# Performance work log

Measured on AMD Instinct MI355X. Metric: run time of the kernel, lower is better.

## Reference

```python
import jax, jax.numpy as jnp
import numpy as np

IMAGE_TOKEN_INDEX = -200
B, N, D = 2, 768, 2048          # batch, seq, llm_size
CLIP = 1024                      # clip hidden size
NUM_HEADS = 8
HEAD_DIM = CLIP // NUM_HEADS
NUM_LAYER, LAYER_RATE = 24, 4
LAYER_IDX = np.asarray(NUM_LAYER - np.arange(0, NUM_LAYER + 1, LAYER_RATE))  # [24,20,16,12,8,4,0]
J = len(LAYER_IDX)               # 7 selected layers
L = NUM_LAYER + 1                # 25 stacked layers in all_features
IMG, PATCH = 336, 14
HP = IMG // PATCH                # 24 patches per side; patch_ratio == 1
HW = HP * HP                     # 576 vision tokens
SL = HP * (HP + 1) + 1           # 601 = H*(W+1)+1 ragged slice length
SCALE = CLIP ** (-0.5)
LN_EPS = 1e-5
COS_EPS = 1e-8


def setup_inputs() -> dict:
    key = jax.random.key(0)
    ks = jax.random.split(key, 10)
    input_ids = jax.random.randint(ks[0], (B, N), 0, 32000)
    pos = jnp.array([37, 111])  # image-token positions; pos + SL <= N
    input_ids = input_ids.at[jnp.arange(B), pos].set(IMAGE_TOKEN_INDEX)
    rgb = jax.random.normal(ks[1], (B, 3, IMG, IMG), dtype=jnp.float32)
    mask = jnp.ones((B, 1, IMG, IMG), dtype=jnp.float32)  # last channel: all-ones mask
    images = jnp.concatenate([rgb, mask], axis=1)
    all_features = jax.random.normal(ks[2], (B, N, L, D), dtype=jnp.float32)
    patch_hw = jnp.full((B, 2), HP, dtype=jnp.int32)
    s = 0.02
    return {
        'input_ids': input_ids,
        'images': images,
        'all_features': all_features,
        'patch_hw': patch_hw,
        'norm_gamma': jnp.ones((J, D), dtype=jnp.float32),
        'norm_beta': jnp.zeros((J, D), dtype=jnp.float32),
        'norm_w': jax.random.normal(ks[3], (J, CLIP, D), dtype=jnp.float32) * s,
        'input_w': jax.random.normal(ks[4], (CLIP, D), dtype=jnp.float32) * s,
        'input_b': jnp.zeros((CLIP,), dtype=jnp.float32),
        'output_w': jax.random.normal(ks[5], (CLIP, CLIP), dtype=jnp.float32) * s,
        'output_b': jnp.zeros((CLIP,), dtype=jnp.float32),
        'clip_w': jax.random.normal(ks[6], (CLIP, 3 * PATCH * PATCH), dtype=jnp.float32) * s,
        'clip_b': jnp.zeros((CLIP,), dtype=jnp.float32),
    }


def reference(input_ids, images, all_features, patch_hw,
              norm_gamma, norm_beta, norm_w,
              input_w, input_b, output_w, output_b, clip_w, clip_b):
    # clip_layer modeled as a frozen 14x14 patch-embed linear -> [B, HW, CLIP]
    patches = images[:, :3].reshape(B, 3, HP, PATCH, HP, PATCH)
    patches = patches.transpose(0, 2, 4, 1, 3, 5).reshape(B, HW, 3 * PATCH * PATCH)
    clip_feats = patches @ clip_w.T + clip_b  # [B, HW, CLIP]
    # mask channel is all ones -> pooled clip_2d_mask keeps every patch
    lidx = jnp.asarray(LAYER_IDX)

    def per_sample(ids, feats, cf):
        # ragged slice at the image token (data-dependent start, fixed length)
        idx = jnp.argmax(ids == IMAGE_TOKEN_INDEX)
        f = jax.lax.dynamic_slice_in_dim(feats, idx, SL, axis=0)[1:]      # [600, L, D]
        # [L,D,H,W+1] drop-last-col in torch == row-major split here
        f = f.reshape(HP, HP + 1, L, D)[:, :HP].reshape(HW, L, D)          # [576, L, D]
        # per-layer LayerNorm + no-bias Linear on 7 selected layers
        xj = f[:, lidx]                                                    # [HW, J, D]
        mu = xj.mean(-1, keepdims=True)
        var = ((xj - mu) ** 2).mean(-1, keepdims=True)
        xn = (xj - mu) / jnp.sqrt(var + LN_EPS) * norm_gamma + norm_beta
        vis = jnp.einsum('njd,jcd->njc', xn, norm_w)                       # [HW, J, CLIP]
        inp = f[:, -1] @ input_w.T + input_b                               # [HW, CLIP]
        # single-query multi-head cross attention over the J-1 kv layers
        q = vis[:, 0].reshape(HW, NUM_HEADS, HEAD_DIM)                     # [HW, h, d]
        kv = vis[:, 1:].reshape(HW, J - 1, NUM_HEADS, HEAD_DIM).transpose(0, 2, 1, 3)  # [HW, h, J-1, d]
        attn = jax.nn.softmax((q[:, :, None, :] * SCALE * kv).sum(-1), axis=-1)        # [HW, h, J-1]
        fuse = (attn[..., None] * kv).sum(-2).reshape(HW, CLIP)
        out = inp + fuse @ output_w.T + output_b                           # [HW, CLIP]
        denom = jnp.maximum(jnp.linalg.norm(out, axis=-1) * jnp.linalg.norm(cf, axis=-1), COS_EPS)
        cos = (out * cf).sum(-1) / denom
        return 1.0 - cos.mean()

    losses = jax.vmap(per_sample)(input_ids, all_features, clip_feats)
    return losses.mean()  # mse_loss / count_image with count_image == B
```

## Files before the change

kernel.cpp:

```cpp
#include <hip/hip_runtime.h>

#define HW_   576
#define BHW   1152
#define DD    2048
#define CLIPC 1024
#define NSEQ  768
#define LL    25
#define KPAD  640

typedef __bf16 bf16x8 __attribute__((ext_vector_type(8)));
typedef float  f32x4  __attribute__((ext_vector_type(4)));
typedef unsigned short u16;

__device__ __forceinline__ float bf2f(u16 u){
  union { unsigned int i; float f; } v; v.i = ((unsigned int)u) << 16; return v.f;
}
__device__ __forceinline__ u16 f2bf(float f){
  union { float f; unsigned int i; } v; v.f = f;
  unsigned int u = v.i;
  return (u16)((u + 0x7fffu + ((u >> 16) & 1u)) >> 16);
}

__device__ __forceinline__ void gld_lds16(const void* g, void* l){
  __builtin_amdgcn_global_load_lds((__attribute__((address_space(1))) void*)g,
                                   (__attribute__((address_space(3))) void*)l,
                                   16, 0, 0);
}

__global__ void setup_k(const int* __restrict__ ids, int* __restrict__ idxbuf,
                        float* __restrict__ rowacc){
  const int lane = threadIdx.x;
  for (int b = 0; b < 2; b++){
    int best = 0x7fffffff;
    for (int i = lane; i < NSEQ; i += 64)
      if (ids[b*NSEQ + i] == -200 && i < best) best = i;
    for (int off = 32; off; off >>= 1){ int o = __shfl_xor(best, off); best = min(best, o); }
    if (lane == 0) idxbuf[b] = best;
  }
  for (int i = lane; i < BHW*4; i += 64) rowacc[i] = 0.f;
}

__global__ void prep_k(const float* __restrict__ norm_w, const float* __restrict__ input_w,
                       const float* __restrict__ output_w, const float* __restrict__ clip_w,
                       const float* __restrict__ images, const float* __restrict__ feats,
                       const int* __restrict__ idxbuf,
                       const float* __restrict__ gamma, const float* __restrict__ beta,
                       u16* __restrict__ B_all, u16* __restrict__ outw,
                       u16* __restrict__ clipw, u16* __restrict__ patch,
                       u16* __restrict__ A_all){
  const int blk = blockIdx.x, tid = threadIdx.x;
  if (blk < 17408){
    const long n1 = 7L*CLIPC*DD, n2 = (long)CLIPC*DD;
    long idx = ((long)blk*256 + tid) * 4;
    const float* s; u16* d;
    if (idx < n1)         { s = norm_w  + idx;              d = B_all + idx; }
    else if (idx < n1+n2) { s = input_w + (idx - n1);       d = B_all + idx; }
    else                  { s = output_w + (idx - n1 - n2); d = outw + (idx - n1 - n2); }
    float4 v = *(const float4*)s;
    union { u16 u[4]; unsigned long long q; } pk;
    pk.u[0] = f2bf(v.x); pk.u[1] = f2bf(v.y); pk.u[2] = f2bf(v.z); pk.u[3] = f2bf(v.w);
    *(unsigned long long*)d = pk.q;
    return;
  }
  if (blk < 18432){
    const int c = blk - 17408;
    for (int k = tid; k < KPAD; k += 256)
      clipw[c*KPAD + k] = (k < 588) ? f2bf(clip_w[c*588 + k]) : (u16)0;
    return;
  }
  if (blk < 19584){
    const int r = blk - 18432;
    const int b = r / HW_, n = r % HW_;
    const int hi = n / 24, wi = n % 24;
    for (int p = tid; p < KPAD; p += 256){
      float v = 0.f;
      if (p < 588){
        int c3 = p / 196, rem = p - c3*196;
        int ph = rem / 14, pw = rem - ph*14;
        v = images[(((long)b*4 + c3)*336 + hi*14 + ph)*336 + wi*14 + pw];
      }
      patch[(long)r*KPAD + p] = f2bf(v);
    }
    return;
  }
  const int q = blk - 19584;
  const int r = q >> 3, g = q & 7;
  const int b = r / HW_, n = r % HW_;
  const int hi = n / 24, wi = n % 24;
  const int tok = idxbuf[b] + 1 + hi*25 + wi;
  const int layer = (g < 7) ? (24 - g*4) : 24;
  const float* src = feats + (((long)(b*NSEQ + tok))*LL + layer)*DD;
  float v[8];
#pragma unroll
  for (int k = 0; k < 8; k++) v[k] = src[tid + k*256];
  u16* dst = A_all + ((long)g*BHW + r)*DD;
  if (g == 7){
#pragma unroll
    for (int k = 0; k < 8; k++) dst[tid + k*256] = f2bf(v[k]);
    return;
  }
  float s = 0.f, qq = 0.f;
#pragma unroll
  for (int k = 0; k < 8; k++){ s += v[k]; qq += v[k]*v[k]; }
  for (int off = 32; off; off >>= 1){ s += __shfl_xor(s, off); qq += __shfl_xor(qq, off); }
  __shared__ float rs[4], rq[4];
  const int wave = tid >> 6, lane = tid & 63;
  if (lane == 0){ rs[wave] = s; rq[wave] = qq; }
  __syncthreads();
  const float ts = rs[0]+rs[1]+rs[2]+rs[3];
  const float tq = rq[0]+rq[1]+rq[2]+rq[3];
  const float mu   = ts * (1.f/2048.f);
  const float var  = tq * (1.f/2048.f) - mu*mu;
  const float rstd = rsqrtf(var + 1e-5f);
  const float* gm = gamma + g*DD;
  const float* bt = beta  + g*DD;
#pragma unroll
  for (int k = 0; k < 8; k++){
    int d = tid + k*256;
    dst[d] = f2bf((v[k]-mu)*rstd*gm[d] + bt[d]);
  }
}

__device__ __forceinline__ void gemm_core(const u16* __restrict__ Az, const u16* __restrict__ Bz,
                                          int K, int bm, int bn,
                                          u16* __restrict__ As, u16* __restrict__ Bs,
                                          f32x4 (&acc)[4][4]){
  const int tid  = threadIdx.x;
  const int wave = tid >> 6, lane = tid & 63;
  const int l15 = lane & 15, quad = lane >> 4;
  const int wr = (wave >> 1) * 64, wc = (wave & 1) * 64;
  const int laneRow = lane >> 3;
  const int laneCol = (((lane & 7) ^ laneRow) * 8);
  const u16* gA = Az + (long)(bm + wave*32 + laneRow)*K + laneCol;
  const u16* gB = Bz + (long)(bn + wave*32 + laneRow)*K + laneCol;
  u16* lA = &As[wave*2048];
  u16* lB = &Bs[wave*2048];
  const long rs8 = (long)8 * K;

  for (int k0 = 0; k0 < K; k0 += 64){
#pragma unroll
    for (int t = 0; t < 4; t++) gld_lds16(gA + k0 + t*rs8, lA + t*512);
#pragma unroll
    for (int t = 0; t < 4; t++) gld_lds16(gB + k0 + t*rs8, lB + t*512);
    __syncthreads();
#pragma unroll
    for (int s = 0; s < 2; s++){
      bf16x8 af[4], bg[4];
#pragma unroll
      for (int i = 0; i < 4; i++)
        af[i] = *(const bf16x8*)&As[(wr + i*16 + l15)*64 + (((s*4 + quad) ^ (l15 & 7)) * 8)];
#pragma unroll
      for (int j = 0; j < 4; j++)
        bg[j] = *(const bf16x8*)&Bs[(wc + j*16 + l15)*64 + (((s*4 + quad) ^ (l15 & 7)) * 8)];
#pragma unroll
      for (int i = 0; i < 4; i++)
#pragma unroll
        for (int j = 0; j < 4; j++)
          acc[i][j] = __builtin_amdgcn_mfma_f32_16x16x32_bf16(af[i], bg[j], acc[i][j], 0, 0, 0);
    }
    __syncthreads();
  }
}

__global__ __launch_bounds__(256, 3)
void gemm9_k(const u16* __restrict__ A_all, const u16* __restrict__ B_all,
             u16* __restrict__ C_all, const u16* __restrict__ patch,
             const u16* __restrict__ clipw, float* __restrict__ cf,
             const float* __restrict__ input_b, const float* __restrict__ clip_b){
  __shared__ alignas(16) u16 As[128*64];
  __shared__ alignas(16) u16 Bs[128*64];
  const int z = blockIdx.z;
  const int bm = blockIdx.x * 128, bn = blockIdx.y * 128;
  const u16 *Az, *Bz; int K;
  if (z < 8){ Az = A_all + (long)z*BHW*DD; Bz = B_all + (long)z*CLIPC*DD; K = DD; }
  else      { Az = patch; Bz = clipw; K = KPAD; }

  f32x4 acc[4][4] = {};
  gemm_core(Az, Bz, K, bm, bn, As, Bs, acc);

  const int lane = threadIdx.x & 63, wave = threadIdx.x >> 6;
  const int l15 = lane & 15, quad = lane >> 4;
  const int wr = (wave >> 1) * 64, wc = (wave & 1) * 64;

  if (z == 8){
#pragma unroll
    for (int i = 0; i < 4; i++)
#pragma unroll
      for (int j = 0; j < 4; j++)
#pragma unroll
        for (int rr = 0; rr < 4; rr++){
          const int row = bm + wr + i*16 + quad*4 + rr;
          const int col = bn + wc + j*16 + l15;
          cf[(long)row*CLIPC + col] = acc[i][j][rr] + clip_b[col];
        }
  } else {
    u16* C = C_all + (long)z*BHW*CLIPC;
    const bool do_bias = (z == 7);
#pragma unroll
    for (int i = 0; i < 4; i++)
#pragma unroll
      for (int j = 0; j < 4; j++)
#pragma unroll
        for (int rr = 0; rr < 4; rr++){
          const int row = bm + wr + i*16 + quad*4 + rr;
          const int col = bn + wc + j*16 + l15;
          float v = acc[i][j][rr];
          if (do_bias) v += input_b[col];
          C[(long)row*CLIPC + col] = f2bf(v);
        }
  }
}

__global__ void attn_k(const u16* __restrict__ C_all, u16* __restrict__ fuse){
  const int r = blockIdx.x;
  const int h = (blockIdx.y << 2) | (threadIdx.x >> 6);
  const int lane = threadIdx.x & 63;
  const long slot = (long)BHW * CLIPC;
  const long rb = (long)r * CLIPC;
  const int c0 = h*128 + lane, c1 = c0 + 64;
  const float q0 = bf2f(C_all[rb + c0]), q1 = bf2f(C_all[rb + c1]);
  float k0v[6], k1v[6], dt[6];
#pragma unroll
  for (int t = 0; t < 6; t++){
    const u16* base = C_all + (long)(t+1)*slot + rb;
    k0v[t] = bf2f(base[c0]); k1v[t] = bf2f(base[c1]);
    dt[t] = q0*k0v[t] + q1*k1v[t];
  }
#pragma unroll
  for (int t = 0; t < 6; t++)
    for (int off = 32; off; off >>= 1) dt[t] += __shfl_xor(dt[t], off);
  float l[6], e[6];
#pragma unroll
  for (int t = 0; t < 6; t++) l[t] = dt[t] * 0.03125f;
  float m = l[0];
#pragma unroll
  for (int t = 1; t < 6; t++) m = fmaxf(m, l[t]);
  float ssum = 0.f;
#pragma unroll
  for (int t = 0; t < 6; t++){ e[t] = __expf(l[t] - m); ssum += e[t]; }
  const float inv = 1.f / ssum;
  float f0 = 0.f, f1 = 0.f;
#pragma unroll
  for (int t = 0; t < 6; t++){ const float a = e[t]*inv; f0 += a*k0v[t]; f1 += a*k1v[t]; }
  fuse[rb + c0] = f2bf(f0);
  fuse[rb + c1] = f2bf(f1);
}

__global__ __launch_bounds__(256, 3)
void gemm_out_k(const u16* __restrict__ fuse, const u16* __restrict__ outw,
                const u16* __restrict__ inp, const float* __restrict__ output_b,
                const float* __restrict__ cf, float* __restrict__ rowacc){
  __shared__ alignas(16) u16 As[128*64];
  __shared__ alignas(16) u16 Bs[128*64];
  const int bm = blockIdx.x * 128, bn = blockIdx.y * 128;
  f32x4 acc[4][4] = {};
  gemm_core(fuse, outw, CLIPC, bm, bn, As, Bs, acc);

  const int lane = threadIdx.x & 63, wave = threadIdx.x >> 6;
  const int l15 = lane & 15, quad = lane >> 4;
  const int wr = (wave >> 1) * 64, wc = (wave & 1) * 64;

#pragma unroll
  for (int i = 0; i < 4; i++)
#pragma unroll
    for (int rr = 0; rr < 4; rr++){
      const int row = bm + wr + i*16 + quad*4 + rr;
      float soc = 0.f, soo = 0.f, scc = 0.f;
#pragma unroll
      for (int j = 0; j < 4; j++){
        const int col = bn + wc + j*16 + l15;
        const long p = (long)row*CLIPC + col;
        const float o = acc[i][j][rr] + output_b[col] + bf2f(inp[p]);
        const float c = cf[p];
        soc += o*c; soo += o*o; scc += c*c;
      }
#pragma unroll
      for (int off = 1; off < 16; off <<= 1){
        soc += __shfl_xor(soc, off); soo += __shfl_xor(soo, off); scc += __shfl_xor(scc, off);
      }
      if (l15 == 0){
        atomicAdd(&rowacc[row*4 + 0], soc);
        atomicAdd(&rowacc[row*4 + 1], soo);
        atomicAdd(&rowacc[row*4 + 2], scc);
      }
    }
}

__global__ void fin_k(const float* __restrict__ rowacc, float* __restrict__ out){
  const int tid = threadIdx.x;
  float s = 0.f;
  for (int r = tid; r < BHW; r += 256){
    const float soc = rowacc[r*4], soo = rowacc[r*4+1], scc = rowacc[r*4+2];
    s += soc / fmaxf(sqrtf(soo*scc), 1e-8f);
  }
  for (int off = 32; off; off >>= 1) s += __shfl_xor(s, off);
  __shared__ float rs[4];
  const int wave = tid >> 6, lane = tid & 63;
  if (lane == 0) rs[wave] = s;
  __syncthreads();
  if (tid == 0) out[0] = 1.f - (rs[0]+rs[1]+rs[2]+rs[3]) * (1.f/(float)BHW);
}

extern "C" void kernel_launch(void* const* d_in, const int* in_sizes, int n_in,
                              void* d_out, int out_size, void* d_ws, size_t ws_size,
                              hipStream_t stream){
  const int*   input_ids = (const int*)  d_in[0];
  const float* images    = (const float*)d_in[1];
  const float* all_feats = (const float*)d_in[2];
  const float* norm_gamma = (const float*)d_in[4];
  const float* norm_beta  = (const float*)d_in[5];
  const float* norm_w     = (const float*)d_in[6];
  const float* input_w    = (const float*)d_in[7];
  const float* input_b    = (const float*)d_in[8];
  const float* output_w   = (const float*)d_in[9];
  const float* output_b   = (const float*)d_in[10];
  const float* clip_w     = (const float*)d_in[11];
  const float* clip_b     = (const float*)d_in[12];
  float* out = (float*)d_out;

  char* w = (char*)d_ws;
  int*   idxbuf = (int*)w;
  size_t off = 256;
  u16* A_all = (u16*)(w + off); off += 8L*BHW*DD*2;
  u16* B_all = (u16*)(w + off); off += 8L*CLIPC*DD*2;
  u16* C_all = (u16*)(w + off); off += 8L*BHW*CLIPC*2;
  u16* outw  = (u16*)(w + off); off += (long)CLIPC*CLIPC*2;
  u16* clipw = (u16*)(w + off); off += (long)CLIPC*KPAD*2;
  u16* patch = (u16*)(w + off); off += (long)BHW*KPAD*2;
  u16* fuse  = (u16*)(w + off); off += (long)BHW*CLIPC*2;
  float* cf     = (float*)(w + off); off += (long)BHW*CLIPC*4;
  float* rowacc = (float*)(w + off); off += (long)BHW*4*4;

  setup_k<<<1, 64, 0, stream>>>(input_ids, idxbuf, rowacc);
  prep_k<<<28800, 256, 0, stream>>>(norm_w, input_w, output_w, clip_w, images, all_feats,
                                    idxbuf, norm_gamma, norm_beta,
                                    B_all, outw, clipw, patch, A_all);
  gemm9_k<<<dim3(9, 8, 9), 256, 0, stream>>>(A_all, B_all, C_all, patch, clipw, cf,
                                             input_b, clip_b);
  attn_k<<<dim3(1152, 2), 256, 0, stream>>>(C_all, fuse);
  gemm_out_k<<<dim3(9, 8), 256, 0, stream>>>(fuse, outw, C_all + 7L*BHW*CLIPC,
                                             output_b, cf, rowacc);
  fin_k<<<1, 256, 0, stream>>>(rowacc, out);
}
```

Measured before the change: 579.9 us.

## Run the seven layer-norm projections as scaled FP8 MFMA GEMMs

```diff
diff --git a/kernel.cpp b/kernel.cpp
--- a/kernel.cpp
+++ b/kernel.cpp
@@ -8,9 +8,15 @@
 #define LL    25
 #define KPAD  640
 
+#define ASCALE 8.0f
+#define BSCALE 32.0f
+#define INV_AB (1.0f/256.0f)
+
 typedef __bf16 bf16x8 __attribute__((ext_vector_type(8)));
 typedef float  f32x4  __attribute__((ext_vector_type(4)));
+typedef int    i32x8  __attribute__((ext_vector_type(8)));
 typedef unsigned short u16;
+typedef unsigned char  u8;
 
 __device__ __forceinline__ float bf2f(u16 u){
   union { unsigned int i; float f; } v; v.i = ((unsigned int)u) << 16; return v.f;
@@ -19,6 +25,15 @@
   union { float f; unsigned int i; } v; v.f = f;
   unsigned int u = v.i;
   return (u16)((u + 0x7fffu + ((u >> 16) & 1u)) >> 16);
+}
+__device__ __forceinline__ unsigned int pk2bf(float a, float b){
+  return ((unsigned int)f2bf(a)) | (((unsigned int)f2bf(b)) << 16);
+}
+__device__ __forceinline__ unsigned int pk4_fp8(float a, float b, float c, float d){
+  int v = 0;
+  v = __builtin_amdgcn_cvt_pk_fp8_f32(a, b, v, false);
+  v = __builtin_amdgcn_cvt_pk_fp8_f32(c, d, v, true);
+  return (unsigned int)v;
 }
 
 __device__ __forceinline__ void gld_lds16(const void* g, void* l){
@@ -45,31 +60,38 @@
                        const float* __restrict__ images, const float* __restrict__ feats,
                        const int* __restrict__ idxbuf,
                        const float* __restrict__ gamma, const float* __restrict__ beta,
-                       u16* __restrict__ B_all, u16* __restrict__ outw,
+                       u8* __restrict__ B8, u16* __restrict__ inpw, u16* __restrict__ outw,
                        u16* __restrict__ clipw, u16* __restrict__ patch,
-                       u16* __restrict__ A_all){
+                       u8* __restrict__ A8, u16* __restrict__ A7){
   const int blk = blockIdx.x, tid = threadIdx.x;
-  if (blk < 17408){
-    const long n1 = 7L*CLIPC*DD, n2 = (long)CLIPC*DD;
-    long idx = ((long)blk*256 + tid) * 4;
-    const float* s; u16* d;
-    if (idx < n1)         { s = norm_w  + idx;              d = B_all + idx; }
-    else if (idx < n1+n2) { s = input_w + (idx - n1);       d = B_all + idx; }
-    else                  { s = output_w + (idx - n1 - n2); d = outw + (idx - n1 - n2); }
-    float4 v = *(const float4*)s;
-    union { u16 u[4]; unsigned long long q; } pk;
-    pk.u[0] = f2bf(v.x); pk.u[1] = f2bf(v.y); pk.u[2] = f2bf(v.z); pk.u[3] = f2bf(v.w);
-    *(unsigned long long*)d = pk.q;
+  if (blk < 7168){
+    long idx = (long)blk*2048 + tid*8;
+    float4 v0 = *(const float4*)(norm_w + idx);
+    float4 v1 = *(const float4*)(norm_w + idx + 4);
+    uint2 o;
+    o.x = pk4_fp8(v0.x*BSCALE, v0.y*BSCALE, v0.z*BSCALE, v0.w*BSCALE);
+    o.y = pk4_fp8(v1.x*BSCALE, v1.y*BSCALE, v1.z*BSCALE, v1.w*BSCALE);
+    *(uint2*)(B8 + idx) = o;
     return;
   }
-  if (blk < 18432){
-    const int c = blk - 17408;
+  if (blk < 8704){
+    const bool isInp = (blk < 8192);
+    long idx = (long)(blk - (isInp ? 7168 : 8192))*2048 + tid*8;
+    const float* s = isInp ? (input_w + idx) : (output_w + idx);
+    float4 v0 = *(const float4*)s;
+    float4 v1 = *(const float4*)(s + 4);
+    uint4 o = { pk2bf(v0.x,v0.y), pk2bf(v0.z,v0.w), pk2bf(v1.x,v1.y), pk2bf(v1.z,v1.w) };
+    *(uint4*)((isInp ? inpw : outw) + idx) = o;
+    return;
+  }
+  if (blk < 9728){
+    const int c = blk - 8704;
     for (int k = tid; k < KPAD; k += 256)
       clipw[c*KPAD + k] = (k < 588) ? f2bf(clip_w[c*588 + k]) : (u16)0;
     return;
   }
-  if (blk < 19584){
-    const int r = blk - 18432;
+  if (blk < 10880){
+    const int r = blk - 9728;
     const int b = r / HW_, n = r % HW_;
     const int hi = n / 24, wi = n % 24;
     for (int p = tid; p < KPAD; p += 256){
@@ -83,25 +105,22 @@
     }
     return;
   }
-  const int q = blk - 19584;
+  const int q = blk - 10880;
   const int r = q >> 3, g = q & 7;
   const int b = r / HW_, n = r % HW_;
   const int hi = n / 24, wi = n % 24;
   const int tok = idxbuf[b] + 1 + hi*25 + wi;
   const int layer = (g < 7) ? (24 - g*4) : 24;
-  const float* src = feats + (((long)(b*NSEQ + tok))*LL + layer)*DD;
-  float v[8];
-#pragma unroll
-  for (int k = 0; k < 8; k++) v[k] = src[tid + k*256];
-  u16* dst = A_all + ((long)g*BHW + r)*DD;
+  const float* src = feats + (((long)(b*NSEQ + tok))*LL + layer)*DD + tid*8;
+  float4 a = *(const float4*)src;
+  float4 c = *(const float4*)(src + 4);
   if (g == 7){
-#pragma unroll
-    for (int k = 0; k < 8; k++) dst[tid + k*256] = f2bf(v[k]);
+    uint4 o = { pk2bf(a.x,a.y), pk2bf(a.z,a.w), pk2bf(c.x,c.y), pk2bf(c.z,c.w) };
+    *(uint4*)(A7 + (long)r*DD + tid*8) = o;
     return;
   }
-  float s = 0.f, qq = 0.f;
-#pragma unroll
-  for (int k = 0; k < 8; k++){ s += v[k]; qq += v[k]*v[k]; }
+  float s  = a.x+a.y+a.z+a.w + c.x+c.y+c.z+c.w;
+  float qq = a.x*a.x+a.y*a.y+a.z*a.z+a.w*a.w + c.x*c.x+c.y*c.y+c.z*c.z+c.w*c.w;
   for (int off = 32; off; off >>= 1){ s += __shfl_xor(s, off); qq += __shfl_xor(qq, off); }
   __shared__ float rs[4], rq[4];
   const int wave = tid >> 6, lane = tid & 63;
@@ -112,13 +131,84 @@
   const float mu   = ts * (1.f/2048.f);
   const float var  = tq * (1.f/2048.f) - mu*mu;
   const float rstd = rsqrtf(var + 1e-5f);
-  const float* gm = gamma + g*DD;
-  const float* bt = beta  + g*DD;
-#pragma unroll
-  for (int k = 0; k < 8; k++){
-    int d = tid + k*256;
-    dst[d] = f2bf((v[k]-mu)*rstd*gm[d] + bt[d]);
-  }
+  const float4 g0 = *(const float4*)(gamma + g*DD + tid*8);
+  const float4 g1 = *(const float4*)(gamma + g*DD + tid*8 + 4);
+  const float4 b0 = *(const float4*)(beta  + g*DD + tid*8);
+  const float4 b1 = *(const float4*)(beta  + g*DD + tid*8 + 4);
+  uint2 o;
+  o.x = pk4_fp8(((a.x-mu)*rstd*g0.x + b0.x)*ASCALE, ((a.y-mu)*rstd*g0.y + b0.y)*ASCALE,
+                ((a.z-mu)*rstd*g0.z + b0.z)*ASCALE, ((a.w-mu)*rstd*g0.w + b0.w)*ASCALE);
+  o.y = pk4_fp8(((c.x-mu)*rstd*g1.x + b1.x)*ASCALE, ((c.y-mu)*rstd*g1.y + b1.y)*ASCALE,
+                ((c.z-mu)*rstd*g1.z + b1.z)*ASCALE, ((c.w-mu)*rstd*g1.w + b1.w)*ASCALE);
+  *(uint2*)(A8 + ((long)g*BHW + r)*DD + tid*8) = o;
+}
+
+__global__ __launch_bounds__(256, 3)
+void gemm_fp8_k(const u8* __restrict__ A_all, const u8* __restrict__ B_all,
+                u16* __restrict__ C_all){
+  __shared__ alignas(16) u8 As[128*128];
+  __shared__ alignas(16) u8 Bs[128*128];
+  const int z = blockIdx.z;
+  const u8* Az = A_all + (long)z*BHW*DD;
+  const u8* Bz = B_all + (long)z*CLIPC*DD;
+  const int bm = blockIdx.x*128, bn = blockIdx.y*128;
+  const int tid = threadIdx.x, wave = tid >> 6, lane = tid & 63;
+  const int l15 = lane & 15, quad = lane >> 4;
+  const int wr = (wave >> 1)*64, wc = (wave & 1)*64;
+  f32x4 acc[4][4] = {};
+
+  const int laneRow   = lane >> 3;
+  const int laneChunk = (lane & 7) ^ laneRow;
+  const u8* gA = Az + (long)(bm + wave*32 + laneRow)*DD + laneChunk*16;
+  const u8* gB = Bz + (long)(bn + wave*32 + laneRow)*DD + laneChunk*16;
+  u8* lA = &As[wave*32*128];
+  u8* lB = &Bs[wave*32*128];
+  const long rs8 = 8L*DD;
+
+  for (int k0 = 0; k0 < DD; k0 += 128){
+#pragma unroll
+    for (int t = 0; t < 4; t++) gld_lds16(gA + k0 + t*rs8, lA + t*1024);
+#pragma unroll
+    for (int t = 0; t < 4; t++) gld_lds16(gB + k0 + t*rs8, lB + t*1024);
+    __syncthreads();
+    i32x8 af[4], bg[4];
+    const int sw = l15 & 7;
+#pragma unroll
+    for (int i = 0; i < 4; i++){
+      const u8* rp = &As[(wr + i*16 + l15)*128];
+      uint4 lo = *(const uint4*)(rp + (((quad*2 + 0) ^ sw)*16));
+      uint4 hi = *(const uint4*)(rp + (((quad*2 + 1) ^ sw)*16));
+      af[i] = (i32x8){(int)lo.x,(int)lo.y,(int)lo.z,(int)lo.w,
+                      (int)hi.x,(int)hi.y,(int)hi.z,(int)hi.w};
+    }
+#pragma unroll
+    for (int j = 0; j < 4; j++){
+      const u8* rp = &Bs[(wc + j*16 + l15)*128];
+      uint4 lo = *(const uint4*)(rp + (((quad*2 + 0) ^ sw)*16));
+      uint4 hi = *(const uint4*)(rp + (((quad*2 + 1) ^ sw)*16));
+      bg[j] = (i32x8){(int)lo.x,(int)lo.y,(int)lo.z,(int)lo.w,
+                      (int)hi.x,(int)hi.y,(int)hi.z,(int)hi.w};
+    }
+#pragma unroll
+    for (int i = 0; i < 4; i++)
+#pragma unroll
+      for (int j = 0; j < 4; j++)
+        acc[i][j] = __builtin_amdgcn_mfma_scale_f32_16x16x128_f8f6f4(
+            af[i], bg[j], acc[i][j], 0, 0, 0, 0x7F7F7F7F, 0, 0x7F7F7F7F);
+    __syncthreads();
+  }
+
+  u16* C = C_all + (long)z*BHW*CLIPC;
+#pragma unroll
+  for (int i = 0; i < 4; i++)
+#pragma unroll
+    for (int j = 0; j < 4; j++)
+#pragma unroll
+      for (int rr = 0; rr < 4; rr++){
+        const int row = bm + wr + i*16 + quad*4 + rr;
+        const int col = bn + wc + j*16 + l15;
+        C[(long)row*CLIPC + col] = f2bf(acc[i][j][rr] * INV_AB);
+      }
 }
 
 __device__ __forceinline__ void gemm_core(const u16* __restrict__ Az, const u16* __restrict__ Bz,
@@ -163,52 +253,34 @@
 }
 
 __global__ __launch_bounds__(256, 3)
-void gemm9_k(const u16* __restrict__ A_all, const u16* __restrict__ B_all,
-             u16* __restrict__ C_all, const u16* __restrict__ patch,
-             const u16* __restrict__ clipw, float* __restrict__ cf,
-             const float* __restrict__ input_b, const float* __restrict__ clip_b){
+void gemm_misc_k(const u16* __restrict__ patch, const u16* __restrict__ clipw,
+                 const u16* __restrict__ A7, const u16* __restrict__ inpw,
+                 float* __restrict__ cf, u16* __restrict__ C7,
+                 const float* __restrict__ clip_b, const float* __restrict__ input_b){
   __shared__ alignas(16) u16 As[128*64];
   __shared__ alignas(16) u16 Bs[128*64];
   const int z = blockIdx.z;
-  const int bm = blockIdx.x * 128, bn = blockIdx.y * 128;
-  const u16 *Az, *Bz; int K;
-  if (z < 8){ Az = A_all + (long)z*BHW*DD; Bz = B_all + (long)z*CLIPC*DD; K = DD; }
-  else      { Az = patch; Bz = clipw; K = KPAD; }
-
+  const int bm = blockIdx.x*128, bn = blockIdx.y*128;
+  const u16* Az = z ? A7 : patch;
+  const u16* Bz = z ? inpw : clipw;
+  const int K = z ? DD : KPAD;
   f32x4 acc[4][4] = {};
   gemm_core(Az, Bz, K, bm, bn, As, Bs, acc);
 
   const int lane = threadIdx.x & 63, wave = threadIdx.x >> 6;
   const int l15 = lane & 15, quad = lane >> 4;
-  const int wr = (wave >> 1) * 64, wc = (wave & 1) * 64;
-
-  if (z == 8){
-#pragma unroll
-    for (int i = 0; i < 4; i++)
-#pragma unroll
-      for (int j = 0; j < 4; j++)
-#pragma unroll
-        for (int rr = 0; rr < 4; rr++){
-          const int row = bm + wr + i*16 + quad*4 + rr;
-          const int col = bn + wc + j*16 + l15;
-          cf[(long)row*CLIPC + col] = acc[i][j][rr] + clip_b[col];
-        }
-  } else {
-    u16* C = C_all + (long)z*BHW*CLIPC;
-    const bool do_bias = (z == 7);
-#pragma unroll
-    for (int i = 0; i < 4; i++)
-#pragma unroll
-      for (int j = 0; j < 4; j++)
-#pragma unroll
-        for (int rr = 0; rr < 4; rr++){
-          const int row = bm + wr + i*16 + quad*4 + rr;
-          const int col = bn + wc + j*16 + l15;
-          float v = acc[i][j][rr];
-          if (do_bias) v += input_b[col];
-          C[(long)row*CLIPC + col] = f2bf(v);
-        }
-  }
+  const int wr = (wave >> 1)*64, wc = (wave & 1)*64;
+#pragma unroll
+  for (int i = 0; i < 4; i++)
+#pragma unroll
+    for (int j = 0; j < 4; j++)
+#pragma unroll
+      for (int rr = 0; rr < 4; rr++){
+        const int row = bm + wr + i*16 + quad*4 + rr;
+        const int col = bn + wc + j*16 + l15;
+        if (z) C7[(long)row*CLIPC + col] = f2bf(acc[i][j][rr] + input_b[col]);
+        else   cf[(long)row*CLIPC + col] = acc[i][j][rr] + clip_b[col];
+      }
 }
 
 __global__ void attn_k(const u16* __restrict__ C_all, u16* __restrict__ fuse){
@@ -252,14 +324,13 @@
                 const float* __restrict__ cf, float* __restrict__ rowacc){
   __shared__ alignas(16) u16 As[128*64];
   __shared__ alignas(16) u16 Bs[128*64];
-  const int bm = blockIdx.x * 128, bn = blockIdx.y * 128;
+  const int bm = blockIdx.x*128, bn = blockIdx.y*128;
   f32x4 acc[4][4] = {};
   gemm_core(fuse, outw, CLIPC, bm, bn, As, Bs, acc);
 
   const int lane = threadIdx.x & 63, wave = threadIdx.x >> 6;
   const int l15 = lane & 15, quad = lane >> 4;
-  const int wr = (wave >> 1) * 64, wc = (wave & 1) * 64;
-
+  const int wr = (wave >> 1)*64, wc = (wave & 1)*64;
 #pragma unroll
   for (int i = 0; i < 4; i++)
 #pragma unroll
@@ -321,22 +392,25 @@
   char* w = (char*)d_ws;
   int*   idxbuf = (int*)w;
   size_t off = 256;
-  u16* A_all = (u16*)(w + off); off += 8L*BHW*DD*2;
-  u16* B_all = (u16*)(w + off); off += 8L*CLIPC*DD*2;
-  u16* C_all = (u16*)(w + off); off += 8L*BHW*CLIPC*2;
+  u8*  A8    = (u8*) (w + off); off += 7L*BHW*DD;
+  u16* A7    = (u16*)(w + off); off += (long)BHW*DD*2;
+  u8*  B8    = (u8*) (w + off); off += 7L*CLIPC*DD;
+  u16* inpw  = (u16*)(w + off); off += (long)CLIPC*DD*2;
   u16* outw  = (u16*)(w + off); off += (long)CLIPC*CLIPC*2;
   u16* clipw = (u16*)(w + off); off += (long)CLIPC*KPAD*2;
   u16* patch = (u16*)(w + off); off += (long)BHW*KPAD*2;
+  u16* C_all = (u16*)(w + off); off += 8L*BHW*CLIPC*2;
   u16* fuse  = (u16*)(w + off); off += (long)BHW*CLIPC*2;
   float* cf     = (float*)(w + off); off += (long)BHW*CLIPC*4;
   float* rowacc = (float*)(w + off); off += (long)BHW*4*4;
 
   setup_k<<<1, 64, 0, stream>>>(input_ids, idxbuf, rowacc);
-  prep_k<<<28800, 256, 0, stream>>>(norm_w, input_w, output_w, clip_w, images, all_feats,
+  prep_k<<<20096, 256, 0, stream>>>(norm_w, input_w, output_w, clip_w, images, all_feats,
                                     idxbuf, norm_gamma, norm_beta,
-                                    B_all, outw, clipw, patch, A_all);
-  gemm9_k<<<dim3(9, 8, 9), 256, 0, stream>>>(A_all, B_all, C_all, patch, clipw, cf,
-                                             input_b, clip_b);
+                                    B8, inpw, outw, clipw, patch, A8, A7);
+  gemm_fp8_k<<<dim3(9, 8, 7), 256, 0, stream>>>(A8, B8, C_all);
+  gemm_misc_k<<<dim3(9, 8, 2), 256, 0, stream>>>(patch, clipw, A7, inpw, cf,
+                                                 C_all + 7L*BHW*CLIPC, clip_b, input_b);
   attn_k<<<dim3(1152, 2), 256, 0, stream>>>(C_all, fuse);
   gemm_out_k<<<dim3(9, 8), 256, 0, stream>>>(fuse, outw, C_all + 7L*BHW*CLIPC,
                                              output_b, cf, rowacc);
```

New measurement: 554.7 us. 1.05x faster.
